# Performance work log

Hardware: AMD Instinct MI355X
Metric: run time of the kernel (lower is better)

## Reference

```python
import jax, jax.numpy as jnp
import numpy as np
import math

D_IN, D_MODEL, N_HEADS, N_LAYERS, D_FF = 128, 256, 4, 4, 1024
NUM_BANDS = D_MODEL // 6  # 42 -> 252 encoding dims, zero-padded to 256
LN_EPS = 1e-5


def setup_inputs() -> dict:
    key = jax.random.key(0)
    ks = jax.random.split(key, 32)
    N, B = 65536, 128
    s = 0.02
    L, D, F = N_LAYERS, D_MODEL, D_FF
    inp = {
        "dom_embeddings": jax.random.normal(ks[0], (N, D_IN), jnp.float32),
        "dom_to_event_idx": jnp.sort(jax.random.randint(ks[1], (N,), 0, B)),
        "batch_size": B,
        "geometry": jax.random.normal(ks[2], (N, 3), jnp.float32),
        "in_proj_w": jax.random.normal(ks[3], (D, D_IN), jnp.float32) * s,
        "in_proj_b": jnp.zeros((D,), jnp.float32),
        "geo_proj_w": jax.random.normal(ks[4], (D, D), jnp.float32) * s,
        "geo_proj_b": jnp.zeros((D,), jnp.float32),
        "cls_token": jax.random.normal(ks[5], (1, 1, D), jnp.float32),
        "qkv_w": jax.random.normal(ks[6], (L, 3 * D, D), jnp.float32) * s,
        "qkv_b": jnp.zeros((L, 3 * D), jnp.float32),
        "out_w": jax.random.normal(ks[7], (L, D, D), jnp.float32) * s,
        "out_b": jnp.zeros((L, D), jnp.float32),
        "ln1_w": jnp.ones((L, D), jnp.float32),
        "ln1_b": jnp.zeros((L, D), jnp.float32),
        "ln2_w": jnp.ones((L, D), jnp.float32),
        "ln2_b": jnp.zeros((L, D), jnp.float32),
        "ff_w1": jax.random.normal(ks[8], (L, F, D), jnp.float32) * s,
        "ff_b1": jnp.zeros((L, F), jnp.float32),
        "ff_w2": jax.random.normal(ks[9], (L, D, F), jnp.float32) * s,
        "ff_b2": jnp.zeros((L, D), jnp.float32),
        "head_w1": jax.random.normal(ks[10], (D, D), jnp.float32) * s,
        "head_b1": jnp.zeros((D,), jnp.float32),
        "head_w2": jax.random.normal(ks[11], (2, D), jnp.float32) * s,
        "head_b2": jnp.zeros((2,), jnp.float32),
    }
    return inp


def _layer_norm(x, w, b):
    m = x.mean(-1, keepdims=True)
    v = ((x - m) ** 2).mean(-1, keepdims=True)
    return (x - m) / jnp.sqrt(v + LN_EPS) * w + b


def _pos_enc(geometry):
    # geometry: (N,3). Order: per coord -> per freq -> [sin, cos]; pad to D_MODEL.
    freqs = jnp.logspace(0.0, 1.0, NUM_BANDS, dtype=jnp.float32)  # 1..max_freq=10
    ang = 2.0 * math.pi * geometry[:, :, None] * freqs[None, None, :]  # (N,3,F)
    sc = jnp.stack([jnp.sin(ang), jnp.cos(ang)], axis=-1)  # (N,3,F,2)
    enc = sc.reshape(geometry.shape[0], 3 * NUM_BANDS * 2)  # (N,252)
    pad = D_MODEL - enc.shape[1]
    return jnp.pad(enc, ((0, 0), (0, pad)))


def _self_attn(x, pad_mask, Wqkv, bqkv, Wo, bo):
    B, S, D = x.shape
    H, hd = N_HEADS, D // N_HEADS
    qkv = x @ Wqkv.T + bqkv  # (B,S,3D)
    q, k, v = jnp.split(qkv, 3, axis=-1)
    q = q.reshape(B, S, H, hd).transpose(0, 2, 1, 3)
    k = k.reshape(B, S, H, hd).transpose(0, 2, 1, 3)
    v = v.reshape(B, S, H, hd).transpose(0, 2, 1, 3)
    scores = jnp.einsum('bhqd,bhkd->bhqk', q, k) / math.sqrt(hd)
    scores = jnp.where(pad_mask[:, None, None, :], -jnp.inf, scores)
    a = jax.nn.softmax(scores, axis=-1)
    o = jnp.einsum('bhqk,bhkd->bhqd', a, v).transpose(0, 2, 1, 3).reshape(B, S, D)
    return o @ Wo.T + bo


def reference(dom_embeddings, dom_to_event_idx, batch_size, geometry,
              in_proj_w, in_proj_b, geo_proj_w, geo_proj_b, cls_token,
              qkv_w, qkv_b, out_w, out_b, ln1_w, ln1_b, ln2_w, ln2_b,
              ff_w1, ff_b1, ff_w2, ff_b2, head_w1, head_b1, head_w2, head_b2):
    N = dom_embeddings.shape[0]
    B = int(batch_size)
    x = dom_embeddings @ in_proj_w.T + in_proj_b  # (N,D)
    geo = _pos_enc(geometry) @ geo_proj_w.T + geo_proj_b
    x = x + geo

    # Vectorized scatter-pack (replaces per-DOM Python loop).
    counts = jnp.bincount(dom_to_event_idx, length=B)
    starts = jnp.concatenate([jnp.zeros((1,), counts.dtype), jnp.cumsum(counts)[:-1]])
    pos = jnp.arange(N) - starts[dom_to_event_idx] + 1  # slot 0 reserved for CLS
    max_doms = int(counts.max())
    S = max_doms + 1

    batch_tensor = jnp.zeros((B, S, D_MODEL), x.dtype)
    batch_tensor = batch_tensor.at[:, 0, :].set(cls_token[0, 0])
    batch_tensor = batch_tensor.at[dom_to_event_idx, pos].set(x)
    # True = padded. NOTE: CLS slot stays True, faithful to original code.
    pad_mask = jnp.ones((B, S), bool).at[dom_to_event_idx, pos].set(False)

    h = batch_tensor
    for l in range(N_LAYERS):  # pre-LN encoder layers
        h = h + _self_attn(_layer_norm(h, ln1_w[l], ln1_b[l]), pad_mask,
                           qkv_w[l], qkv_b[l], out_w[l], out_b[l])
        ff_in = _layer_norm(h, ln2_w[l], ln2_b[l])
        h = h + jax.nn.relu(ff_in @ ff_w1[l].T + ff_b1[l]) @ ff_w2[l].T + ff_b2[l]

    cls = h[:, 0, :]
    hid = jax.nn.relu(cls @ head_w1.T + head_b1)
    return hid @ head_w2.T + head_b2  # (B,2)
```

## Files before the change

### kernel.cpp

```cpp
#include <hip/hip_runtime.h>
#include <hip/hip_bf16.h>
#include <math.h>


#define D_INPUT  128
#define DM       256
#define NHEADS   4
#define HDIM     64
#define NLAYERS  4
#define DFF      1024
#define BEV      128
#define LNEPS    1e-5f
#define KT       10
#define SCL      0.18033688011112042f

typedef unsigned short u16;
typedef __attribute__((ext_vector_type(8))) short bf16x8;
typedef __attribute__((ext_vector_type(4))) float f32x4;

__device__ inline u16 f2bf(float x) {
    unsigned int xi = __float_as_uint(x);
    unsigned int r  = xi + 0x7FFFu + ((xi >> 16) & 1u);
    return (u16)(r >> 16);
}
__device__ inline unsigned int cvtpk(float lo, float hi) {
    unsigned int r;
    asm("v_cvt_pk_bf16_f32 %0, %1, %2" : "=v"(r) : "v"(lo), "v"(hi));
    return r;
}
__device__ inline void gload16(const void* g, void* l) {
    __builtin_amdgcn_global_load_lds(
        (const __attribute__((address_space(1))) unsigned int*)g,
        (__attribute__((address_space(3))) unsigned int*)l, 16, 0, 0);
}

__device__ inline size_t wpack_off(int col, int k, int nkt) {
    const int c16 = col >> 4, llo = col & 15;
    const int kt = k >> 6, kr = k & 63;
    const int kk = kr >> 5, lhi = (kr >> 3) & 3, e = kr & 7;
    return ((size_t)(c16 * nkt + kt)) * 1024 + kk * 512 + (lhi * 16 + llo) * 8 + e;
}


__global__ void starts_kernel(const int* __restrict__ idx, int* __restrict__ counts,
                              int* __restrict__ starts, int N) {
    __shared__ int bnd[BEV + 1];
    const int b = threadIdx.x;
    if (b <= BEV) {
        int lo = 0, hi = N;
        while (lo < hi) { int mid = (lo + hi) >> 1; if (idx[mid] < b) lo = mid + 1; else hi = mid; }
        bnd[b] = lo;
    }
    __syncthreads();
    if (b < BEV) { starts[b] = bnd[b]; counts[b] = bnd[b + 1] - bnd[b]; }
}

__global__ void r2bs_kernel(const int* __restrict__ idx, const int* __restrict__ starts,
                            int* __restrict__ r2bs, int N, int TP) {
    int i = blockIdx.x * blockDim.x + threadIdx.x;
    if (i < N) {
        int b = idx[i];
        r2bs[i] = (b << 16) | (i - starts[b] + 1);
    } else if (i < N + BEV) {
        r2bs[i] = (i - N) << 16;
    } else if (i < TP) {
        r2bs[i] = BEV << 16;
    }
}

__global__ void beacon_kernel(float* out, int n, float v) {
    int i = blockIdx.x * blockDim.x + threadIdx.x;
    if (i < n) out[i] = v;
}

__global__ void cvt4p_kernel(const float* __restrict__ s0, const float* __restrict__ s1,
                             const float* __restrict__ s2, const float* __restrict__ s3,
                             u16* __restrict__ d0, u16* __restrict__ d1,
                             u16* __restrict__ d2, u16* __restrict__ d3) {
    const int n0 = NLAYERS * 768 * 256, n1 = NLAYERS * 256 * 256;
    const int n2 = NLAYERS * 1024 * 256, n3 = NLAYERS * 256 * 1024;
    int i = blockIdx.x * blockDim.x + threadIdx.x;
    if (i < n0) {
        const int NoK = 768 * 256;
        int l = i / NoK, rem = i - l * NoK, col = rem >> 8, k = rem & 255;
        d0[(size_t)l * NoK + wpack_off(col, k, 4)] = f2bf(s0[i]);
        return;
    }
    i -= n0;
    if (i < n1) {
        const int NoK = 256 * 256;
        int l = i / NoK, rem = i - l * NoK, col = rem >> 8, k = rem & 255;
        d1[(size_t)l * NoK + wpack_off(col, k, 4)] = f2bf(s1[i]);
        return;
    }
    i -= n1;
    if (i < n2) {
        const int NoK = 1024 * 256;
        int l = i / NoK, rem = i - l * NoK, col = rem >> 8, k = rem & 255;
        d2[(size_t)l * NoK + wpack_off(col, k, 4)] = f2bf(s2[i]);
        return;
    }
    i -= n2;
    if (i < n3) {
        const int NoK = 256 * 1024;
        int l = i / NoK, rem = i - l * NoK, col = rem >> 10, k = rem & 1023;
        d3[(size_t)l * NoK + wpack_off(col, k, 16)] = f2bf(s3[i]);
    }
}

__global__ void prep_w_kernel(const float* __restrict__ win, const float* __restrict__ wgeo,
                              const float* __restrict__ bin, const float* __restrict__ bgeo,
                              u16* __restrict__ We, float* __restrict__ be) {
    int i = blockIdx.x * blockDim.x + threadIdx.x;
    if (i < 256 * 384) {
        int o = i / 384, k = i % 384;
        float v = 0.f;
        if (k < 128)      v = win[o * 128 + k];
        else if (k < 380) v = wgeo[o * 256 + (k - 128)];
        We[wpack_off(o, k, 6)] = f2bf(v);
    }
    if (i < 256) be[i] = bin[i] + bgeo[i];
}

__global__ void prep_a_kernel(const float* __restrict__ emb, const float* __restrict__ geo,
                              u16* __restrict__ A, int N) {
    size_t i = (size_t)blockIdx.x * blockDim.x + threadIdx.x;
    if (i >= (size_t)N * 384) return;
    int k = (int)(i % 384);
    size_t r = i / 384;
    float v = 0.f;
    if (k < 128) {
        v = emb[r * 128 + k];
    } else if (k < 380) {
        int rem  = k - 128;
        int axis = rem / 84;
        int r2   = rem % 84;
        int band = r2 >> 1;
        int sc   = r2 & 1;
        float freq = expf((float)band * (2.3025850929940457f / 41.0f));
        float ang  = (6.283185307179586f * geo[r * 3 + axis]) * freq;
        v = sc ? cosf(ang) : sinf(ang);
    }
    A[i] = f2bf(v);
}

__global__ void cls_kernel(const float* __restrict__ cls, float* __restrict__ h, int N) {
    h[(size_t)(N + blockIdx.x) * DM + threadIdx.x] = cls[threadIdx.x];
}


__global__ __launch_bounds__(256) void ln_kernel(const float* __restrict__ x,
                                                 const float* __restrict__ w,
                                                 const float* __restrict__ b,
                                                 u16* __restrict__ y, int T) {
    int row  = blockIdx.x * 4 + (threadIdx.x >> 6);
    int lane = threadIdx.x & 63;
    if (row >= T) return;
    float4 v = ((const float4*)(x + (size_t)row * DM))[lane];
    float s = v.x + v.y + v.z + v.w;
    #pragma unroll
    for (int off = 32; off > 0; off >>= 1) s += __shfl_xor(s, off);
    float mean = s * (1.0f / 256.0f);
    float dx = v.x - mean, dy = v.y - mean, dz = v.z - mean, dw = v.w - mean;
    float ss = dx * dx + dy * dy + dz * dz + dw * dw;
    #pragma unroll
    for (int off = 32; off > 0; off >>= 1) ss += __shfl_xor(ss, off);
    float inv = rsqrtf(ss * (1.0f / 256.0f) + LNEPS);
    float4 wv = ((const float4*)w)[lane];
    float4 bv = ((const float4*)b)[lane];
    ushort4 o;
    o.x = f2bf(dx * inv * wv.x + bv.x);
    o.y = f2bf(dy * inv * wv.y + bv.y);
    o.z = f2bf(dz * inv * wv.z + bv.z);
    o.w = f2bf(dw * inv * wv.w + bv.w);
    ((ushort4*)(y + (size_t)row * DM))[lane] = o;
}


template <typename OutT>
__global__ __launch_bounds__(512) void mgemm_kernel(const u16* __restrict__ A,
                                                    const u16* __restrict__ Wp,
                                                    const float* __restrict__ bias,
                                                    OutT* __restrict__ C,
                                                    int K, int No, int ldc, int flags,
                                                    const int* __restrict__ r2bs,
                                                    u16* __restrict__ KVt) {
    __shared__ u16 As[256 * 64];
    const int m0 = blockIdx.y * 256, n0 = blockIdx.x * 128;
    const int tid  = threadIdx.x;
    const int w    = tid >> 6, lane = tid & 63;
    const int wr   = w >> 1,  wc   = w & 1;
    const int lhi  = lane >> 4, llo = lane & 15;
    const int nkt  = K >> 6;

    f32x4 acc[4][4];
    #pragma unroll
    for (int i = 0; i < 4; ++i)
        #pragma unroll
        for (int j = 0; j < 4; ++j) acc[i][j] = (f32x4){0.f, 0.f, 0.f, 0.f};

    for (int kt = 0; kt < K; kt += 64) {
        __syncthreads();
        #pragma unroll
        for (int it = 0; it < 4; ++it) {
            int un = it * 512 + tid;
            int r = un >> 3, c8 = un & 7;
            gload16(A + (size_t)(m0 + r) * K + kt + ((c8 ^ (r & 7)) * 8), &As[un * 8]);
        }
        __syncthreads();
        const u16* wb = Wp + ((size_t)(kt >> 6)) * 1024 + lane * 8;
        #pragma unroll
        for (int kk = 0; kk < 2; ++kk) {
            bf16x8 af[4], bfr[4];
            #pragma unroll
            for (int i = 0; i < 4; ++i) {
                const int row = wr * 64 + i * 16 + llo;
                af[i] = *(const bf16x8*)&As[row * 64 + (((kk * 4 + lhi) ^ (row & 7)) * 8)];
            }
            #pragma unroll
            for (int j = 0; j < 4; ++j) {
                const int c16 = (n0 >> 4) + wc * 4 + j;
                bfr[j] = *(const bf16x8*)(wb + ((size_t)c16 * nkt) * 1024 + kk * 512);
            }
            #pragma unroll
            for (int i = 0; i < 4; ++i)
                #pragma unroll
                for (int j = 0; j < 4; ++j)
                    acc[i][j] = __builtin_amdgcn_mfma_f32_16x16x32_bf16(af[i], bfr[j], acc[i][j], 0, 0, 0);
        }
    }

    const int vmode = (flags & 4) ? (n0 >= 512 ? 2 : (n0 >= 256 ? 1 : 0)) : 0;
    #pragma unroll
    for (int i = 0; i < 4; ++i) {
        const int row0 = m0 + wr * 64 + i * 16 + lhi * 4;
        int bsr[4];
        if (vmode) {
            #pragma unroll
            for (int r = 0; r < 4; ++r) bsr[r] = r2bs[row0 + r];
        }
        #pragma unroll
        for (int j = 0; j < 4; ++j) {
            const int col = n0 + wc * 64 + j * 16 + llo;
            const float bb = bias[col];
            if (vmode == 1) {
                const int hh = (col - 256) >> 6, d = (col - 256) & 63;
                const int kk_t = d >> 5, lhi_t = (d >> 3) & 3, e = d & 7;
                #pragma unroll
                for (int r = 0; r < 4; ++r) {
                    const int eb = bsr[r] >> 16, pos = bsr[r] & 0xffff;
                    const int ktile = pos >> 6;
                    if (ktile < KT) {
                        const int unit = ((pos & 63) >> 4) * 2 + kk_t;
                        const int lane_t = lhi_t * 16 + (pos & 15);
                        KVt[(((size_t)(eb * 4 + hh) * 2 + 0) * KT + ktile) * 4096
                            + unit * 512 + lane_t * 8 + e] = f2bf(acc[i][j][r] + bb);
                    }
                }
            } else if (vmode == 2) {
                const int hh = (col - 512) >> 6, d = (col - 512) & 63;
                const int i_t = d >> 4, llo_t = d & 15;
                #pragma unroll
                for (int r = 0; r < 4; ++r) {
                    const int eb = bsr[r] >> 16, pos = bsr[r] & 0xffff;
                    const int ktile = pos >> 6;
                    if (ktile < KT) {
                        const int unit = i_t * 2 + ((pos & 63) >> 5);
                        const int lane_t = (((pos & 63) >> 3) & 3) * 16 + llo_t;
                        KVt[(((size_t)(eb * 4 + hh) * 2 + 1) * KT + ktile) * 4096
                            + unit * 512 + lane_t * 8 + (pos & 7)] = f2bf(acc[i][j][r] + bb);
                    }
                }
            } else {
                #pragma unroll
                for (int r = 0; r < 4; ++r) {
                    float v = acc[i][j][r] + bb;
                    if ((flags & 8) && col < 256) v *= SCL;
                    size_t idx = (size_t)(row0 + r) * ldc + col;
                    if constexpr (sizeof(OutT) == 4) {
                        float* cp = (float*)C + idx;
                        if (flags & 2) v += *cp;
                        if (flags & 1) v = fmaxf(v, 0.f);
                        *cp = v;
                    } else {
                        if (flags & 1) v = fmaxf(v, 0.f);
                        ((u16*)C)[idx] = f2bf(v);
                    }
                }
            }
        }
    }
}


__global__ __launch_bounds__(256) void mgemmln_kernel(const u16* __restrict__ X,
                                                      const u16* __restrict__ Wp,
                                                      const float* __restrict__ bias,
                                                      float* __restrict__ H,
                                                      const float* __restrict__ lnw,
                                                      const float* __restrict__ lnb,
                                                      u16* __restrict__ Y,
                                                      int K) {
    __shared__ u16 Xs[64 * 64];
    __shared__ float part[2][4][64];
    const int m0 = blockIdx.x * 64;
    const int tid = threadIdx.x;
    const int wc = tid >> 6, lane = tid & 63;
    const int lhi = lane >> 4, llo = lane & 15;
    const int nkt = K >> 6;

    f32x4 acc[4][4];
    #pragma unroll
    for (int i = 0; i < 4; ++i)
        #pragma unroll
        for (int j = 0; j < 4; ++j) acc[i][j] = (f32x4){0.f, 0.f, 0.f, 0.f};

    for (int kt = 0; kt < K; kt += 64) {
        __syncthreads();
        #pragma unroll
        for (int it = 0; it < 2; ++it) {
            int un = it * 256 + tid;
            int r = un >> 3, c8 = un & 7;
            gload16(X + (size_t)(m0 + r) * K + kt + ((c8 ^ (r & 7)) * 8), &Xs[un * 8]);
        }
        __syncthreads();
        const u16* wb = Wp + ((size_t)(kt >> 6)) * 1024 + lane * 8;
        #pragma unroll
        for (int kk = 0; kk < 2; ++kk) {
            bf16x8 xf[4], wf[4];
            #pragma unroll
            for (int i = 0; i < 4; ++i) {
                const int row = i * 16 + llo;
                xf[i] = *(const bf16x8*)&Xs[row * 64 + (((kk * 4 + lhi) ^ (row & 7)) * 8)];
            }
            #pragma unroll
            for (int j = 0; j < 4; ++j) {
                const int c16 = wc * 4 + j;
                wf[j] = *(const bf16x8*)(wb + ((size_t)c16 * nkt) * 1024 + kk * 512);
            }
            #pragma unroll
            for (int i = 0; i < 4; ++i)
                #pragma unroll
                for (int j = 0; j < 4; ++j)
                    acc[i][j] = __builtin_amdgcn_mfma_f32_16x16x32_bf16(wf[j], xf[i], acc[i][j], 0, 0, 0);
        }
    }

    float rsum[4], rsq[4];
    #pragma unroll
    for (int i = 0; i < 4; ++i) { rsum[i] = 0.f; rsq[i] = 0.f; }
    #pragma unroll
    for (int i = 0; i < 4; ++i) {
        const int row = m0 + i * 16 + llo;
        #pragma unroll
        for (int j = 0; j < 4; ++j) {
            const int col0 = wc * 64 + j * 16 + lhi * 4;
            const float4 bb = *(const float4*)&bias[col0];
            const float4 hv = *(const float4*)&H[(size_t)row * DM + col0];
            float v0 = acc[i][j][0] + bb.x + hv.x;
            float v1 = acc[i][j][1] + bb.y + hv.y;
            float v2 = acc[i][j][2] + bb.z + hv.z;
            float v3 = acc[i][j][3] + bb.w + hv.w;
            acc[i][j][0] = v0; acc[i][j][1] = v1; acc[i][j][2] = v2; acc[i][j][3] = v3;
            rsum[i] += (v0 + v1) + (v2 + v3);
            rsq[i]  += (v0 * v0 + v1 * v1) + (v2 * v2 + v3 * v3);
        }
    }
    #pragma unroll
    for (int i = 0; i < 4; ++i) {
        rsum[i] += __shfl_xor(rsum[i], 16);  rsum[i] += __shfl_xor(rsum[i], 32);
        rsq[i]  += __shfl_xor(rsq[i], 16);   rsq[i]  += __shfl_xor(rsq[i], 32);
    }
    __syncthreads();
    if (lhi == 0) {
        #pragma unroll
        for (int i = 0; i < 4; ++i) {
            const int rl = i * 16 + llo;
            part[0][wc][rl] = rsum[i];
            part[1][wc][rl] = rsq[i];
        }
    }
    __syncthreads();

    #pragma unroll
    for (int i = 0; i < 4; ++i) {
        const int rl = i * 16 + llo;
        const int row = m0 + rl;
        const float s = (part[0][0][rl] + part[0][1][rl]) + (part[0][2][rl] + part[0][3][rl]);
        const float q = (part[1][0][rl] + part[1][1][rl]) + (part[1][2][rl] + part[1][3][rl]);
        const float mean = s * (1.0f / 256.0f);
        const float var  = fmaxf(q * (1.0f / 256.0f) - mean * mean, 0.f);
        const float rstd = rsqrtf(var + LNEPS);
        #pragma unroll
        for (int j = 0; j < 4; ++j) {
            const int col0 = wc * 64 + j * 16 + lhi * 4;
            const float4 wv = *(const float4*)&lnw[col0];
            const float4 bv = *(const float4*)&lnb[col0];
            float4 hv;
            hv.x = acc[i][j][0]; hv.y = acc[i][j][1];
            hv.z = acc[i][j][2]; hv.w = acc[i][j][3];
            *(float4*)&H[(size_t)row * DM + col0] = hv;
            uint2 yy;
            yy.x = cvtpk((hv.x - mean) * rstd * wv.x + bv.x,
                         (hv.y - mean) * rstd * wv.y + bv.y);
            yy.y = cvtpk((hv.z - mean) * rstd * wv.z + bv.z,
                         (hv.w - mean) * rstd * wv.w + bv.w);
            *(uint2*)&Y[(size_t)row * DM + col0] = yy;
        }
    }
}


__global__ __launch_bounds__(256) void mattn_kernel(const u16* __restrict__ Qb,
                                                    const u16* __restrict__ KVt,
                                                    const int* __restrict__ counts,
                                                    const int* __restrict__ starts,
                                                    u16* __restrict__ out, int N) {
    const int id  = blockIdx.x;
    const int rem = id >> 3;
    const int qt  = rem % KT;
    const int bh  = (rem / KT) * 8 + (id & 7);
    const int b = bh >> 2, hh = bh & 3;
    const int Sb = counts[b] + 1;
    const int qbase = qt * 64;
    if (qbase >= Sb) return;
    const int start = starts[b];
    __shared__ u16 Pl[4][16 * 72];
    const int tid = threadIdx.x;
    const int w = tid >> 6, lane = tid & 63;
    const int llo = lane & 15, lhi = lane >> 4;

    const int qi = qbase + w * 16 + llo;
    const size_t qrow = (qi < Sb && qi > 0) ? (size_t)(start + qi - 1) : (size_t)(N + b);
    bf16x8 bq[2];
    bq[0] = *(const bf16x8*)(Qb + qrow * 256 + hh * 64 + lhi * 8);
    bq[1] = *(const bf16x8*)(Qb + qrow * 256 + hh * 64 + 32 + lhi * 8);

    const u16* kb = KVt + ((size_t)bh * 2 + 0) * KT * 4096;
    const u16* vb = KVt + ((size_t)bh * 2 + 1) * KT * 4096;

    f32x4 acc[4];
    #pragma unroll
    for (int i = 0; i < 4; ++i) acc[i] = (f32x4){0.f, 0.f, 0.f, 0.f};
    float m = -1e30f, l = 0.f;

    int nt = (Sb + 63) >> 6;
    if (nt > KT) nt = KT;

    for (int t = 0; t < nt; ++t) {
        const int kbase = t * 64;
        const u16* kp = kb + t * 4096 + lane * 8;
        const u16* vp = vb + t * 4096 + lane * 8;

        bf16x8 ak[4][2], av[4][2];
        #pragma unroll
        for (int i = 0; i < 4; ++i) {
            #pragma unroll
            for (int kk = 0; kk < 2; ++kk) {
                ak[i][kk] = *(const bf16x8*)(kp + (i * 2 + kk) * 512);
                av[i][kk] = *(const bf16x8*)(vp + (i * 2 + kk) * 512);
            }
        }

        f32x4 sc[4];
        #pragma unroll
        for (int i = 0; i < 4; ++i) sc[i] = (f32x4){0.f, 0.f, 0.f, 0.f};
        #pragma unroll
        for (int kk = 0; kk < 2; ++kk)
            #pragma unroll
            for (int i = 0; i < 4; ++i)
                sc[i] = __builtin_amdgcn_mfma_f32_16x16x32_bf16(ak[i][kk], bq[kk], sc[i], 0, 0, 0);

        float rm;
        if (kbase + 64 <= Sb) {
            float m0v = fmaxf(fmaxf(sc[0][0], sc[0][1]), fmaxf(sc[0][2], sc[0][3]));
            float m1v = fmaxf(fmaxf(sc[1][0], sc[1][1]), fmaxf(sc[1][2], sc[1][3]));
            float m2v = fmaxf(fmaxf(sc[2][0], sc[2][1]), fmaxf(sc[2][2], sc[2][3]));
            float m3v = fmaxf(fmaxf(sc[3][0], sc[3][1]), fmaxf(sc[3][2], sc[3][3]));
            rm = fmaxf(fmaxf(m0v, m1v), fmaxf(m2v, m3v));
        } else {
            rm = -1e30f;
            #pragma unroll
            for (int i = 0; i < 4; ++i)
                #pragma unroll
                for (int r = 0; r < 4; ++r) {
                    const int key = kbase + i * 16 + lhi * 4 + r;
                    const float s = (key < Sb) ? sc[i][r] : -1e30f;
                    sc[i][r] = s;
                    rm = fmaxf(rm, s);
                }
        }
        rm = fmaxf(rm, __shfl_xor(rm, 16));
        rm = fmaxf(rm, __shfl_xor(rm, 32));

        if (!__all(rm <= m + 8.f)) {
            const float mnew = fmaxf(m, rm);
            const float corr = exp2f(m - mnew);
            l *= corr;
            #pragma unroll
            for (int i = 0; i < 4; ++i) acc[i] *= corr;
            m = mnew;
        }

        float ls = 0.f;
        #pragma unroll
        for (int i = 0; i < 4; ++i) {
            const float p0 = exp2f(sc[i][0] - m), p1 = exp2f(sc[i][1] - m);
            const float p2 = exp2f(sc[i][2] - m), p3 = exp2f(sc[i][3] - m);
            ls += (p0 + p1) + (p2 + p3);
            uint2 pp;
            pp.x = cvtpk(p0, p1);
            pp.y = cvtpk(p2, p3);
            *(uint2*)&Pl[w][llo * 72 + i * 16 + lhi * 4] = pp;
        }
        ls += __shfl_xor(ls, 16);
        ls += __shfl_xor(ls, 32);
        l += ls;

        #pragma unroll
        for (int kk = 0; kk < 2; ++kk) {
            bf16x8 pb = *(const bf16x8*)&Pl[w][llo * 72 + kk * 32 + lhi * 8];
            #pragma unroll
            for (int i = 0; i < 4; ++i)
                acc[i] = __builtin_amdgcn_mfma_f32_16x16x32_bf16(av[i][kk], pb, acc[i], 0, 0, 0);
        }
    }

    if (qi < Sb) {
        const size_t orow = (qi == 0) ? (size_t)(N + b) : (size_t)(start + qi - 1);
        const float invl = 1.f / l;
        #pragma unroll
        for (int i = 0; i < 4; ++i) {
            ushort4 o;
            o.x = f2bf(acc[i][0] * invl);
            o.y = f2bf(acc[i][1] * invl);
            o.z = f2bf(acc[i][2] * invl);
            o.w = f2bf(acc[i][3] * invl);
            *(ushort4*)&out[orow * DM + hh * HDIM + i * 16 + lhi * 4] = o;
        }
    }
}


__global__ __launch_bounds__(256) void head_kernel(const float* __restrict__ h,
                                                   const float* __restrict__ w1,
                                                   const float* __restrict__ b1,
                                                   const float* __restrict__ w2,
                                                   const float* __restrict__ b2,
                                                   float* __restrict__ out, int N) {
    const int b = blockIdx.x;
    const int t = threadIdx.x;
    __shared__ float cls[DM];
    __shared__ float hid[DM];
    cls[t] = h[(size_t)(N + b) * DM + t];
    __syncthreads();
    float s = b1[t];
    for (int k = 0; k < DM; ++k) s = fmaf(cls[k], w1[t * DM + k], s);
    hid[t] = fmaxf(s, 0.f);
    __syncthreads();
    if (t < 2) {
        float o = b2[t];
        for (int k = 0; k < DM; ++k) o = fmaf(hid[k], w2[t * DM + k], o);
        out[b * 2 + t] = o;
    }
}


extern "C" void kernel_launch(void* const* d_in, const int* in_sizes, int n_in,
                              void* d_out, int out_size, void* d_ws, size_t ws_size,
                              hipStream_t stream) {
    const float* dom_emb   = (const float*)d_in[0];
    const int*   dom_idx   = (const int*)d_in[1];
    const float* geometry  = (const float*)d_in[3];
    const float* in_w      = (const float*)d_in[4];
    const float* in_b      = (const float*)d_in[5];
    const float* geo_w     = (const float*)d_in[6];
    const float* geo_b     = (const float*)d_in[7];
    const float* cls_tok   = (const float*)d_in[8];
    const float* qkv_w     = (const float*)d_in[9];
    const float* qkv_b     = (const float*)d_in[10];
    const float* out_w     = (const float*)d_in[11];
    const float* out_b     = (const float*)d_in[12];
    const float* ln1_w     = (const float*)d_in[13];
    const float* ln1_b     = (const float*)d_in[14];
    const float* ln2_w     = (const float*)d_in[15];
    const float* ln2_b     = (const float*)d_in[16];
    const float* ff_w1     = (const float*)d_in[17];
    const float* ff_b1     = (const float*)d_in[18];
    const float* ff_w2     = (const float*)d_in[19];
    const float* ff_b2     = (const float*)d_in[20];
    const float* head_w1   = (const float*)d_in[21];
    const float* head_b1   = (const float*)d_in[22];
    const float* head_w2   = (const float*)d_in[23];
    const float* head_b2   = (const float*)d_in[24];
    float* outp = (float*)d_out;

    const int N  = in_sizes[0] / D_INPUT;
    const int T  = N + BEV;
    const int TP = ((T + 255) / 256) * 256;

    char* base = (char*)d_ws;
    size_t off = 0;
    int* counts = (int*)(base + off);          off += 1024;
    int* starts = (int*)(base + off);          off += 1024;
    u16*   Web  = (u16*)(base + off);          off += (size_t)256 * 384 * 2;
    float* be   = (float*)(base + off);        off += 1024;
    u16*   wq   = (u16*)(base + off);          off += (size_t)NLAYERS * 768 * 256 * 2;
    u16*   wo   = (u16*)(base + off);          off += (size_t)NLAYERS * 256 * 256 * 2;
    u16*   w1b  = (u16*)(base + off);          off += (size_t)NLAYERS * 1024 * 256 * 2;
    u16*   w2b  = (u16*)(base + off);          off += (size_t)NLAYERS * 256 * 1024 * 2;
    int*   r2bs = (int*)(base + off);          off += ((size_t)TP * 4 + 255) & ~255ULL;
    float* h    = (float*)(base + off);        off += (size_t)TP * DM * 4;
    u16*   xb   = (u16*)(base + off);          off += (size_t)TP * DM * 2;
    const size_t qb_sz  = (size_t)TP * 256 * 2;
    const size_t kvt_sz = (size_t)(BEV + 1) * 4 * 2 * KT * 4096 * 2;
    const size_t big2   = qb_sz + kvt_sz;
    const size_t ff1_sz = (size_t)TP * 1024 * 2;
    char* bigc = base + off;
    const bool ff_single = ws_size >= off + (ff1_sz > big2 ? ff1_sz : big2);
    off += ff_single ? (ff1_sz > big2 ? ff1_sz : big2) : big2;

    u16* Ab   = (u16*)bigc;
    u16* Qbuf = (u16*)bigc;
    u16* KVt  = (u16*)(bigc + qb_sz);
    u16* ffm  = (u16*)bigc;

    if (ws_size < off) {
        beacon_kernel<<<1, 256, 0, stream>>>(outp, out_size, (float)(ws_size >> 20));
        return;
    }

    {
        const int ntot = NLAYERS * (768 * 256 + 256 * 256 + 1024 * 256 + 256 * 1024);
        cvt4p_kernel<<<(ntot + 255) / 256, 256, 0, stream>>>(
            qkv_w, out_w, ff_w1, ff_w2, wq, wo, w1b, w2b);
    }
    prep_w_kernel<<<(256 * 384 + 255) / 256, 256, 0, stream>>>(in_w, geo_w, in_b, geo_b, Web, be);

    starts_kernel<<<1, 256, 0, stream>>>(dom_idx, counts, starts, N);
    r2bs_kernel<<<(TP + 255) / 256, 256, 0, stream>>>(dom_idx, starts, r2bs, N, TP);

    prep_a_kernel<<<(int)(((size_t)N * 384 + 255) / 256), 256, 0, stream>>>(dom_emb, geometry, Ab, N);
    mgemm_kernel<float><<<dim3(2, N / 256), 512, 0, stream>>>(
        Ab, Web, be, h, 384, DM, DM, 0, nullptr, nullptr);
    cls_kernel<<<BEV, DM, 0, stream>>>(cls_tok, h, N);

    const int MT = TP / 256;
    int chs[2], nch;
    if (ff_single) { chs[0] = MT; nch = 1; }
    else           { chs[0] = (MT + 1) / 2; chs[1] = MT - chs[0]; nch = 2; }
    ln_kernel<<<TP / 4, 256, 0, stream>>>(h, ln1_w, ln1_b, xb, TP);
    for (int l = 0; l < NLAYERS; ++l) {
        mgemm_kernel<u16><<<dim3(6, MT), 512, 0, stream>>>(
            xb, wq + (size_t)l * 768 * 256, qkv_b + l * 768, Qbuf, 256, 768, 256, 4 | 8,
            r2bs, KVt);
        mattn_kernel<<<8 * KT * (BEV * NHEADS / 8), 256, 0, stream>>>(
            Qbuf, KVt, counts, starts, xb, N);
        mgemmln_kernel<<<TP / 64, 256, 0, stream>>>(
            xb, wo + (size_t)l * 256 * 256, out_b + l * DM, h,
            ln2_w + l * DM, ln2_b + l * DM, xb, 256);
        const int lnx = (l + 1 < NLAYERS) ? (l + 1) : l;
        int t0 = 0;
        for (int c = 0; c < nch; ++c) {
            const size_t r0 = (size_t)t0 * 256;
            mgemm_kernel<u16><<<dim3(8, chs[c]), 512, 0, stream>>>(
                xb + r0 * DM, w1b + (size_t)l * DFF * 256, ff_b1 + l * DFF, ffm,
                256, DFF, DFF, 1, nullptr, nullptr);
            mgemmln_kernel<<<chs[c] * 4, 256, 0, stream>>>(
                ffm, w2b + (size_t)l * 256 * DFF, ff_b2 + l * DM, h + r0 * DM,
                ln1_w + lnx * DM, ln1_b + lnx * DM, xb + r0 * DM, DFF);
            t0 += chs[c];
        }
    }

    head_kernel<<<BEV, DM, 0, stream>>>(h, head_w1, head_b1, head_w2, head_b2, outp, N);
}
```

Baseline: 1.762 ms.

## Pre-pack activations in MFMA tile layout and fuse the feed-forward block into one kernel

Activations are now written straight into the MFMA fragment-packed layout (apack), so the GEMMs read fragments directly from global memory and no longer stage tiles through LDS or synchronise around them. The FF1 and FF2 GEMMs are fused into one kernel that keeps the 1024-wide intermediate on chip, which removes the large round trip of the intermediate buffer and the chunking logic. The QKV GEMM is rewritten with smaller row tiles and vectorised epilogue stores, the input kernel packs four values per thread, and attention MFMA sections get s_setprio hints. Dropping LDS staging puts more load on L2/global bandwidth, and the fused FF kernel may have lower occupancy.

Measured after the change: 2.805 ms. 1.59x slower.

```diff
diff --git a/kernel.cpp b/kernel.cpp
--- a/kernel.cpp
+++ b/kernel.cpp
@@ -28,12 +28,12 @@
     asm("v_cvt_pk_bf16_f32 %0, %1, %2" : "=v"(r) : "v"(lo), "v"(hi));
     return r;
 }
-__device__ inline void gload16(const void* g, void* l) {
-    __builtin_amdgcn_global_load_lds(
-        (const __attribute__((address_space(1))) unsigned int*)g,
-        (__attribute__((address_space(3))) unsigned int*)l, 16, 0, 0);
-}
-
+
+__device__ inline size_t apack(int row, int col, int nkt) {
+    return ((size_t)(row >> 4) * nkt + (col >> 6)) * 1024
+         + ((col >> 5) & 1) * 512
+         + ((((col >> 3) & 3) * 16 + (row & 15)) * 8) + (col & 7);
+}
 __device__ inline size_t wpack_off(int col, int k, int nkt) {
     const int c16 = col >> 4, llo = col & 15;
     const int kt = k >> 6, kr = k & 63;
@@ -123,25 +123,34 @@
 }
 
 __global__ void prep_a_kernel(const float* __restrict__ emb, const float* __restrict__ geo,
-                              u16* __restrict__ A, int N) {
-    size_t i = (size_t)blockIdx.x * blockDim.x + threadIdx.x;
-    if (i >= (size_t)N * 384) return;
-    int k = (int)(i % 384);
-    size_t r = i / 384;
-    float v = 0.f;
-    if (k < 128) {
-        v = emb[r * 128 + k];
-    } else if (k < 380) {
-        int rem  = k - 128;
-        int axis = rem / 84;
-        int r2   = rem % 84;
-        int band = r2 >> 1;
-        int sc   = r2 & 1;
-        float freq = expf((float)band * (2.3025850929940457f / 41.0f));
-        float ang  = (6.283185307179586f * geo[r * 3 + axis]) * freq;
-        v = sc ? cosf(ang) : sinf(ang);
-    }
-    A[i] = f2bf(v);
+                              u16* __restrict__ Ap, int N) {
+    size_t t = (size_t)blockIdx.x * blockDim.x + threadIdx.x;
+    if (t >= (size_t)N * 96) return;
+    const int c4 = (int)(t % 96) * 4;
+    const size_t r = t / 96;
+    float v[4];
+    #pragma unroll
+    for (int u = 0; u < 4; ++u) {
+        const int k = c4 + u;
+        float x = 0.f;
+        if (k < 128) {
+            x = emb[r * 128 + k];
+        } else if (k < 380) {
+            int rem  = k - 128;
+            int axis = rem / 84;
+            int r2   = rem % 84;
+            int band = r2 >> 1;
+            int sc   = r2 & 1;
+            float freq = expf((float)band * (2.3025850929940457f / 41.0f));
+            float ang  = (6.283185307179586f * geo[r * 3 + axis]) * freq;
+            x = sc ? cosf(ang) : sinf(ang);
+        }
+        v[u] = x;
+    }
+    uint2 pp;
+    pp.x = cvtpk(v[0], v[1]);
+    pp.y = cvtpk(v[2], v[3]);
+    *(uint2*)&Ap[apack((int)r, c4, 6)] = pp;
 }
 
 __global__ void cls_kernel(const float* __restrict__ cls, float* __restrict__ h, int N) {
@@ -152,7 +161,7 @@
 __global__ __launch_bounds__(256) void ln_kernel(const float* __restrict__ x,
                                                  const float* __restrict__ w,
                                                  const float* __restrict__ b,
-                                                 u16* __restrict__ y, int T) {
+                                                 u16* __restrict__ yp, int T) {
     int row  = blockIdx.x * 4 + (threadIdx.x >> 6);
     int lane = threadIdx.x & 63;
     if (row >= T) return;
@@ -168,30 +177,27 @@
     float inv = rsqrtf(ss * (1.0f / 256.0f) + LNEPS);
     float4 wv = ((const float4*)w)[lane];
     float4 bv = ((const float4*)b)[lane];
-    ushort4 o;
-    o.x = f2bf(dx * inv * wv.x + bv.x);
-    o.y = f2bf(dy * inv * wv.y + bv.y);
-    o.z = f2bf(dz * inv * wv.z + bv.z);
-    o.w = f2bf(dw * inv * wv.w + bv.w);
-    ((ushort4*)(y + (size_t)row * DM))[lane] = o;
-}
-
-
-template <typename OutT>
-__global__ __launch_bounds__(512) void mgemm_kernel(const u16* __restrict__ A,
+    const int col0 = lane * 4;
+    uint2 yy;
+    yy.x = cvtpk(dx * inv * wv.x + bv.x, dy * inv * wv.y + bv.y);
+    yy.y = cvtpk(dz * inv * wv.z + bv.z, dw * inv * wv.w + bv.w);
+    *(uint2*)&yp[apack(row, col0, 4)] = yy;
+}
+
+
+template <int MODE>
+__global__ __launch_bounds__(256) void pgemm_kernel(const u16* __restrict__ Xp,
                                                     const u16* __restrict__ Wp,
                                                     const float* __restrict__ bias,
-                                                    OutT* __restrict__ C,
-                                                    int K, int No, int ldc, int flags,
+                                                    float* __restrict__ C,
+                                                    u16* __restrict__ Qb,
+                                                    u16* __restrict__ KVt,
                                                     const int* __restrict__ r2bs,
-                                                    u16* __restrict__ KVt) {
-    __shared__ u16 As[256 * 64];
-    const int m0 = blockIdx.y * 256, n0 = blockIdx.x * 128;
-    const int tid  = threadIdx.x;
-    const int w    = tid >> 6, lane = tid & 63;
-    const int wr   = w >> 1,  wc   = w & 1;
-    const int lhi  = lane >> 4, llo = lane & 15;
-    const int nkt  = K >> 6;
+                                                    int nkt) {
+    const int m0 = blockIdx.y * 64, n0 = blockIdx.x * 256;
+    const int tid = threadIdx.x, wv = tid >> 6, lane = tid & 63;
+    const int lhi = lane >> 4, llo = lane & 15;
+    const int rt0 = m0 >> 4;
 
     f32x4 acc[4][4];
     #pragma unroll
@@ -199,93 +205,69 @@
         #pragma unroll
         for (int j = 0; j < 4; ++j) acc[i][j] = (f32x4){0.f, 0.f, 0.f, 0.f};
 
-    for (int kt = 0; kt < K; kt += 64) {
-        __syncthreads();
-        #pragma unroll
-        for (int it = 0; it < 4; ++it) {
-            int un = it * 512 + tid;
-            int r = un >> 3, c8 = un & 7;
-            gload16(A + (size_t)(m0 + r) * K + kt + ((c8 ^ (r & 7)) * 8), &As[un * 8]);
-        }
-        __syncthreads();
-        const u16* wb = Wp + ((size_t)(kt >> 6)) * 1024 + lane * 8;
+    for (int kt = 0; kt < nkt; ++kt) {
         #pragma unroll
         for (int kk = 0; kk < 2; ++kk) {
-            bf16x8 af[4], bfr[4];
-            #pragma unroll
-            for (int i = 0; i < 4; ++i) {
-                const int row = wr * 64 + i * 16 + llo;
-                af[i] = *(const bf16x8*)&As[row * 64 + (((kk * 4 + lhi) ^ (row & 7)) * 8)];
-            }
+            bf16x8 xf[4], wf[4];
+            #pragma unroll
+            for (int i = 0; i < 4; ++i)
+                xf[i] = *(const bf16x8*)(Xp + ((size_t)(rt0 + i) * nkt + kt) * 1024
+                                         + kk * 512 + lane * 8);
             #pragma unroll
             for (int j = 0; j < 4; ++j) {
-                const int c16 = (n0 >> 4) + wc * 4 + j;
-                bfr[j] = *(const bf16x8*)(wb + ((size_t)c16 * nkt) * 1024 + kk * 512);
+                const int c16 = (n0 >> 4) + wv * 4 + j;
+                wf[j] = *(const bf16x8*)(Wp + ((size_t)c16 * nkt + kt) * 1024
+                                         + kk * 512 + lane * 8);
             }
             #pragma unroll
             for (int i = 0; i < 4; ++i)
                 #pragma unroll
                 for (int j = 0; j < 4; ++j)
-                    acc[i][j] = __builtin_amdgcn_mfma_f32_16x16x32_bf16(af[i], bfr[j], acc[i][j], 0, 0, 0);
-        }
-    }
-
-    const int vmode = (flags & 4) ? (n0 >= 512 ? 2 : (n0 >= 256 ? 1 : 0)) : 0;
+                    acc[i][j] = __builtin_amdgcn_mfma_f32_16x16x32_bf16(wf[j], xf[i], acc[i][j], 0, 0, 0);
+        }
+    }
+
     #pragma unroll
     for (int i = 0; i < 4; ++i) {
-        const int row0 = m0 + wr * 64 + i * 16 + lhi * 4;
-        int bsr[4];
-        if (vmode) {
-            #pragma unroll
-            for (int r = 0; r < 4; ++r) bsr[r] = r2bs[row0 + r];
+        const int row = m0 + i * 16 + llo;
+        int eb = 0, pos = 0, ktile = KT;
+        if (MODE == 1 && n0 >= 256) {
+            const int bs = r2bs[row];
+            eb = bs >> 16; pos = bs & 0xffff; ktile = pos >> 6;
         }
         #pragma unroll
         for (int j = 0; j < 4; ++j) {
-            const int col = n0 + wc * 64 + j * 16 + llo;
-            const float bb = bias[col];
-            if (vmode == 1) {
-                const int hh = (col - 256) >> 6, d = (col - 256) & 63;
-                const int kk_t = d >> 5, lhi_t = (d >> 3) & 3, e = d & 7;
-                #pragma unroll
-                for (int r = 0; r < 4; ++r) {
-                    const int eb = bsr[r] >> 16, pos = bsr[r] & 0xffff;
-                    const int ktile = pos >> 6;
-                    if (ktile < KT) {
-                        const int unit = ((pos & 63) >> 4) * 2 + kk_t;
-                        const int lane_t = lhi_t * 16 + (pos & 15);
-                        KVt[(((size_t)(eb * 4 + hh) * 2 + 0) * KT + ktile) * 4096
-                            + unit * 512 + lane_t * 8 + e] = f2bf(acc[i][j][r] + bb);
-                    }
-                }
-            } else if (vmode == 2) {
-                const int hh = (col - 512) >> 6, d = (col - 512) & 63;
-                const int i_t = d >> 4, llo_t = d & 15;
-                #pragma unroll
-                for (int r = 0; r < 4; ++r) {
-                    const int eb = bsr[r] >> 16, pos = bsr[r] & 0xffff;
-                    const int ktile = pos >> 6;
-                    if (ktile < KT) {
-                        const int unit = i_t * 2 + ((pos & 63) >> 5);
-                        const int lane_t = (((pos & 63) >> 3) & 3) * 16 + llo_t;
-                        KVt[(((size_t)(eb * 4 + hh) * 2 + 1) * KT + ktile) * 4096
-                            + unit * 512 + lane_t * 8 + (pos & 7)] = f2bf(acc[i][j][r] + bb);
-                    }
+            const int col0 = n0 + wv * 64 + j * 16 + lhi * 4;
+            const float4 bb = *(const float4*)&bias[col0];
+            const float v0 = acc[i][j][0] + bb.x, v1 = acc[i][j][1] + bb.y;
+            const float v2 = acc[i][j][2] + bb.z, v3 = acc[i][j][3] + bb.w;
+            if (MODE == 0) {
+                float4 c = {v0, v1, v2, v3};
+                *(float4*)&C[(size_t)row * 256 + col0] = c;
+            } else if (n0 == 0) {
+                uint2 q;
+                q.x = cvtpk(v0 * SCL, v1 * SCL);
+                q.y = cvtpk(v2 * SCL, v3 * SCL);
+                *(uint2*)&Qb[(size_t)row * 256 + col0] = q;
+            } else if (n0 == 256) {
+                if (ktile < KT) {
+                    const int dg = col0 - 256, hh = dg >> 6, d0 = dg & 63;
+                    const int unit = ((pos & 63) >> 4) * 2 + (d0 >> 5);
+                    const int lt = ((d0 >> 3) & 3) * 16 + (pos & 15);
+                    uint2 pp = {cvtpk(v0, v1), cvtpk(v2, v3)};
+                    *(uint2*)&KVt[(((size_t)(eb * 4 + hh) * 2 + 0) * KT + ktile) * 4096
+                                  + unit * 512 + lt * 8 + (d0 & 7)] = pp;
                 }
             } else {
-                #pragma unroll
-                for (int r = 0; r < 4; ++r) {
-                    float v = acc[i][j][r] + bb;
-                    if ((flags & 8) && col < 256) v *= SCL;
-                    size_t idx = (size_t)(row0 + r) * ldc + col;
-                    if constexpr (sizeof(OutT) == 4) {
-                        float* cp = (float*)C + idx;
-                        if (flags & 2) v += *cp;
-                        if (flags & 1) v = fmaxf(v, 0.f);
-                        *cp = v;
-                    } else {
-                        if (flags & 1) v = fmaxf(v, 0.f);
-                        ((u16*)C)[idx] = f2bf(v);
-                    }
+                if (ktile < KT) {
+                    const int dg = col0 - 512, hh = dg >> 6, d0 = dg & 63;
+                    const size_t vb = (((size_t)(eb * 4 + hh) * 2 + 1) * KT + ktile) * 4096
+                                    + ((d0 >> 4) * 2 + ((pos & 63) >> 5)) * 512
+                                    + ((((pos & 63) >> 3) & 3) * 16) * 8 + (pos & 7);
+                    KVt[vb + (size_t)((d0 & 15) + 0) * 8] = f2bf(v0);
+                    KVt[vb + (size_t)((d0 & 15) + 1) * 8] = f2bf(v1);
+                    KVt[vb + (size_t)((d0 & 15) + 2) * 8] = f2bf(v2);
+                    KVt[vb + (size_t)((d0 & 15) + 3) * 8] = f2bf(v3);
                 }
             }
         }
@@ -293,21 +275,19 @@
 }
 
 
-__global__ __launch_bounds__(256) void mgemmln_kernel(const u16* __restrict__ X,
+__global__ __launch_bounds__(256) void mgemmln_kernel(const u16* __restrict__ Xp,
                                                       const u16* __restrict__ Wp,
                                                       const float* __restrict__ bias,
                                                       float* __restrict__ H,
                                                       const float* __restrict__ lnw,
                                                       const float* __restrict__ lnb,
-                                                      u16* __restrict__ Y,
-                                                      int K) {
-    __shared__ u16 Xs[64 * 64];
+                                                      u16* __restrict__ Yp,
+                                                      int nkt) {
     __shared__ float part[2][4][64];
     const int m0 = blockIdx.x * 64;
-    const int tid = threadIdx.x;
-    const int wc = tid >> 6, lane = tid & 63;
+    const int tid = threadIdx.x, wv = tid >> 6, lane = tid & 63;
     const int lhi = lane >> 4, llo = lane & 15;
-    const int nkt = K >> 6;
+    const int rt0 = m0 >> 4;
 
     f32x4 acc[4][4];
     #pragma unroll
@@ -315,28 +295,19 @@
         #pragma unroll
         for (int j = 0; j < 4; ++j) acc[i][j] = (f32x4){0.f, 0.f, 0.f, 0.f};
 
-    for (int kt = 0; kt < K; kt += 64) {
-        __syncthreads();
-        #pragma unroll
-        for (int it = 0; it < 2; ++it) {
-            int un = it * 256 + tid;
-            int r = un >> 3, c8 = un & 7;
-            gload16(X + (size_t)(m0 + r) * K + kt + ((c8 ^ (r & 7)) * 8), &Xs[un * 8]);
-        }
-        __syncthreads();
-        const u16* wb = Wp + ((size_t)(kt >> 6)) * 1024 + lane * 8;
+    for (int kt = 0; kt < nkt; ++kt) {
         #pragma unroll
         for (int kk = 0; kk < 2; ++kk) {
             bf16x8 xf[4], wf[4];
             #pragma unroll
-            for (int i = 0; i < 4; ++i) {
-                const int row = i * 16 + llo;
-                xf[i] = *(const bf16x8*)&Xs[row * 64 + (((kk * 4 + lhi) ^ (row & 7)) * 8)];
-            }
+            for (int i = 0; i < 4; ++i)
+                xf[i] = *(const bf16x8*)(Xp + ((size_t)(rt0 + i) * nkt + kt) * 1024
+                                         + kk * 512 + lane * 8);
             #pragma unroll
             for (int j = 0; j < 4; ++j) {
-                const int c16 = wc * 4 + j;
-                wf[j] = *(const bf16x8*)(wb + ((size_t)c16 * nkt) * 1024 + kk * 512);
+                const int c16 = wv * 4 + j;
+                wf[j] = *(const bf16x8*)(Wp + ((size_t)c16 * nkt + kt) * 1024
+                                         + kk * 512 + lane * 8);
             }
             #pragma unroll
             for (int i = 0; i < 4; ++i)
@@ -354,7 +325,7 @@
         const int row = m0 + i * 16 + llo;
         #pragma unroll
         for (int j = 0; j < 4; ++j) {
-            const int col0 = wc * 64 + j * 16 + lhi * 4;
+            const int col0 = wv * 64 + j * 16 + lhi * 4;
             const float4 bb = *(const float4*)&bias[col0];
             const float4 hv = *(const float4*)&H[(size_t)row * DM + col0];
             float v0 = acc[i][j][0] + bb.x + hv.x;
@@ -376,8 +347,8 @@
         #pragma unroll
         for (int i = 0; i < 4; ++i) {
             const int rl = i * 16 + llo;
-            part[0][wc][rl] = rsum[i];
-            part[1][wc][rl] = rsq[i];
+            part[0][wv][rl] = rsum[i];
+            part[1][wv][rl] = rsq[i];
         }
     }
     __syncthreads();
@@ -393,19 +364,163 @@
         const float rstd = rsqrtf(var + LNEPS);
         #pragma unroll
         for (int j = 0; j < 4; ++j) {
-            const int col0 = wc * 64 + j * 16 + lhi * 4;
-            const float4 wv = *(const float4*)&lnw[col0];
-            const float4 bv = *(const float4*)&lnb[col0];
+            const int col0 = wv * 64 + j * 16 + lhi * 4;
+            const float4 wl = *(const float4*)&lnw[col0];
+            const float4 bl = *(const float4*)&lnb[col0];
             float4 hv;
             hv.x = acc[i][j][0]; hv.y = acc[i][j][1];
             hv.z = acc[i][j][2]; hv.w = acc[i][j][3];
             *(float4*)&H[(size_t)row * DM + col0] = hv;
             uint2 yy;
-            yy.x = cvtpk((hv.x - mean) * rstd * wv.x + bv.x,
-                         (hv.y - mean) * rstd * wv.y + bv.y);
-            yy.y = cvtpk((hv.z - mean) * rstd * wv.z + bv.z,
-                         (hv.w - mean) * rstd * wv.w + bv.w);
-            *(uint2*)&Y[(size_t)row * DM + col0] = yy;
+            yy.x = cvtpk((hv.x - mean) * rstd * wl.x + bl.x,
+                         (hv.y - mean) * rstd * wl.y + bl.y);
+            yy.y = cvtpk((hv.z - mean) * rstd * wl.z + bl.z,
+                         (hv.w - mean) * rstd * wl.w + bl.w);
+            *(uint2*)&Yp[apack(row, col0, 4)] = yy;
+        }
+    }
+}
+
+
+__global__ __launch_bounds__(512) void fusedff_kernel(const u16* __restrict__ Xp,
+                                                      const u16* __restrict__ W1p,
+                                                      const float* __restrict__ b1,
+                                                      const u16* __restrict__ W2p,
+                                                      const float* __restrict__ b2,
+                                                      float* __restrict__ H,
+                                                      const float* __restrict__ lnw,
+                                                      const float* __restrict__ lnb,
+                                                      u16* __restrict__ Yp) {
+    __shared__ u16 mid[8 * 8 * 2 * 512];
+    __shared__ float part[2][8][128];
+    const int m0 = blockIdx.x * 128;
+    const int tid = threadIdx.x, wv = tid >> 6, lane = tid & 63;
+    const int lhi = lane >> 4, llo = lane & 15;
+    const int rt0 = m0 >> 4;
+
+    f32x4 oacc[8][2];
+    #pragma unroll
+    for (int i = 0; i < 8; ++i)
+        #pragma unroll
+        for (int j = 0; j < 2; ++j) oacc[i][j] = (f32x4){0.f, 0.f, 0.f, 0.f};
+
+    for (int h2 = 0; h2 < 2; ++h2) {
+        for (int j2 = 0; j2 < 4; ++j2) {
+            const int c16 = h2 * 32 + wv * 4 + j2;
+            f32x4 acc[8];
+            #pragma unroll
+            for (int i = 0; i < 8; ++i) acc[i] = (f32x4){0.f, 0.f, 0.f, 0.f};
+            for (int kt = 0; kt < 4; ++kt) {
+                const u16* wb = W1p + ((size_t)(c16 * 4 + kt)) * 1024 + lane * 8;
+                #pragma unroll
+                for (int kk = 0; kk < 2; ++kk) {
+                    bf16x8 wf = *(const bf16x8*)(wb + kk * 512);
+                    #pragma unroll
+                    for (int i = 0; i < 8; ++i) {
+                        bf16x8 xf = *(const bf16x8*)(Xp + ((size_t)(rt0 + i) * 4 + kt) * 1024
+                                                     + kk * 512 + lane * 8);
+                        acc[i] = __builtin_amdgcn_mfma_f32_16x16x32_bf16(wf, xf, acc[i], 0, 0, 0);
+                    }
+                }
+            }
+            const int colbase = c16 * 16 + lhi * 4;
+            const float4 bb = *(const float4*)&b1[colbase];
+            const int mtH = (colbase >> 6) - h2 * 8;
+            const int kk2 = (colbase >> 5) & 1;
+            const int lt  = ((colbase >> 3) & 3) * 16 + llo;
+            const int e0  = colbase & 7;
+            #pragma unroll
+            for (int i = 0; i < 8; ++i) {
+                const float v0 = fmaxf(acc[i][0] + bb.x, 0.f);
+                const float v1 = fmaxf(acc[i][1] + bb.y, 0.f);
+                const float v2 = fmaxf(acc[i][2] + bb.z, 0.f);
+                const float v3 = fmaxf(acc[i][3] + bb.w, 0.f);
+                uint2 pp = {cvtpk(v0, v1), cvtpk(v2, v3)};
+                *(uint2*)&mid[((i * 8 + mtH) * 2 + kk2) * 512 + lt * 8 + e0] = pp;
+            }
+        }
+        __syncthreads();
+        for (int mtH = 0; mtH < 8; ++mtH) {
+            #pragma unroll
+            for (int kk = 0; kk < 2; ++kk) {
+                bf16x8 mf[8];
+                #pragma unroll
+                for (int i = 0; i < 8; ++i)
+                    mf[i] = *(const bf16x8*)&mid[((i * 8 + mtH) * 2 + kk) * 512 + lane * 8];
+                #pragma unroll
+                for (int j = 0; j < 2; ++j) {
+                    const int c16o = wv * 2 + j;
+                    bf16x8 wf = *(const bf16x8*)(W2p + ((size_t)(c16o * 16 + h2 * 8 + mtH)) * 1024
+                                                 + kk * 512 + lane * 8);
+                    #pragma unroll
+                    for (int i = 0; i < 8; ++i)
+                        oacc[i][j] = __builtin_amdgcn_mfma_f32_16x16x32_bf16(wf, mf[i], oacc[i][j], 0, 0, 0);
+                }
+            }
+        }
+        __syncthreads();
+    }
+
+    float rsum[8], rsq[8];
+    #pragma unroll
+    for (int i = 0; i < 8; ++i) { rsum[i] = 0.f; rsq[i] = 0.f; }
+    #pragma unroll
+    for (int i = 0; i < 8; ++i) {
+        const int row = m0 + i * 16 + llo;
+        #pragma unroll
+        for (int j = 0; j < 2; ++j) {
+            const int col0 = wv * 32 + j * 16 + lhi * 4;
+            const float4 bb = *(const float4*)&b2[col0];
+            const float4 hv = *(const float4*)&H[(size_t)row * DM + col0];
+            float v0 = oacc[i][j][0] + bb.x + hv.x;
+            float v1 = oacc[i][j][1] + bb.y + hv.y;
+            float v2 = oacc[i][j][2] + bb.z + hv.z;
+            float v3 = oacc[i][j][3] + bb.w + hv.w;
+            oacc[i][j][0] = v0; oacc[i][j][1] = v1; oacc[i][j][2] = v2; oacc[i][j][3] = v3;
+            rsum[i] += (v0 + v1) + (v2 + v3);
+            rsq[i]  += (v0 * v0 + v1 * v1) + (v2 * v2 + v3 * v3);
+        }
+    }
+    #pragma unroll
+    for (int i = 0; i < 8; ++i) {
+        rsum[i] += __shfl_xor(rsum[i], 16);  rsum[i] += __shfl_xor(rsum[i], 32);
+        rsq[i]  += __shfl_xor(rsq[i], 16);   rsq[i]  += __shfl_xor(rsq[i], 32);
+    }
+    if (lhi == 0) {
+        #pragma unroll
+        for (int i = 0; i < 8; ++i) {
+            const int rl = i * 16 + llo;
+            part[0][wv][rl] = rsum[i];
+            part[1][wv][rl] = rsq[i];
+        }
+    }
+    __syncthreads();
+
+    #pragma unroll
+    for (int i = 0; i < 8; ++i) {
+        const int rl = i * 16 + llo;
+        const int row = m0 + rl;
+        float s = 0.f, q = 0.f;
+        #pragma unroll
+        for (int w2 = 0; w2 < 8; ++w2) { s += part[0][w2][rl]; q += part[1][w2][rl]; }
+        const float mean = s * (1.0f / 256.0f);
+        const float var  = fmaxf(q * (1.0f / 256.0f) - mean * mean, 0.f);
+        const float rstd = rsqrtf(var + LNEPS);
+        #pragma unroll
+        for (int j = 0; j < 2; ++j) {
+            const int col0 = wv * 32 + j * 16 + lhi * 4;
+            const float4 wl = *(const float4*)&lnw[col0];
+            const float4 bl = *(const float4*)&lnb[col0];
+            float4 hv;
+            hv.x = oacc[i][j][0]; hv.y = oacc[i][j][1];
+            hv.z = oacc[i][j][2]; hv.w = oacc[i][j][3];
+            *(float4*)&H[(size_t)row * DM + col0] = hv;
+            uint2 yy;
+            yy.x = cvtpk((hv.x - mean) * rstd * wl.x + bl.x,
+                         (hv.y - mean) * rstd * wl.y + bl.y);
+            yy.y = cvtpk((hv.z - mean) * rstd * wl.z + bl.z,
+                         (hv.w - mean) * rstd * wl.w + bl.w);
+            *(uint2*)&Yp[apack(row, col0, 4)] = yy;
         }
     }
 }
@@ -415,7 +530,7 @@
                                                     const u16* __restrict__ KVt,
                                                     const int* __restrict__ counts,
                                                     const int* __restrict__ starts,
-                                                    u16* __restrict__ out, int N) {
+                                                    u16* __restrict__ outp, int N) {
     const int id  = blockIdx.x;
     const int rem = id >> 3;
     const int qt  = rem % KT;
@@ -465,11 +580,13 @@
         f32x4 sc[4];
         #pragma unroll
         for (int i = 0; i < 4; ++i) sc[i] = (f32x4){0.f, 0.f, 0.f, 0.f};
+        __builtin_amdgcn_s_setprio(1);
         #pragma unroll
         for (int kk = 0; kk < 2; ++kk)
             #pragma unroll
             for (int i = 0; i < 4; ++i)
                 sc[i] = __builtin_amdgcn_mfma_f32_16x16x32_bf16(ak[i][kk], bq[kk], sc[i], 0, 0, 0);
+        __builtin_amdgcn_s_setprio(0);
 
         float rm;
         if (kbase + 64 <= Sb) {
@@ -517,6 +634,7 @@
         ls += __shfl_xor(ls, 32);
         l += ls;
 
+        __builtin_amdgcn_s_setprio(1);
         #pragma unroll
         for (int kk = 0; kk < 2; ++kk) {
             bf16x8 pb = *(const bf16x8*)&Pl[w][llo * 72 + kk * 32 + lhi * 8];
@@ -524,6 +642,7 @@
             for (int i = 0; i < 4; ++i)
                 acc[i] = __builtin_amdgcn_mfma_f32_16x16x32_bf16(av[i][kk], pb, acc[i], 0, 0, 0);
         }
+        __builtin_amdgcn_s_setprio(0);
     }
 
     if (qi < Sb) {
@@ -531,12 +650,11 @@
         const float invl = 1.f / l;
         #pragma unroll
         for (int i = 0; i < 4; ++i) {
-            ushort4 o;
-            o.x = f2bf(acc[i][0] * invl);
-            o.y = f2bf(acc[i][1] * invl);
-            o.z = f2bf(acc[i][2] * invl);
-            o.w = f2bf(acc[i][3] * invl);
-            *(ushort4*)&out[orow * DM + hh * HDIM + i * 16 + lhi * 4] = o;
+            const int col0 = hh * 64 + i * 16 + lhi * 4;
+            uint2 yy;
+            yy.x = cvtpk(acc[i][0] * invl, acc[i][1] * invl);
+            yy.y = cvtpk(acc[i][2] * invl, acc[i][3] * invl);
+            *(uint2*)&outp[apack((int)orow, col0, 4)] = yy;
         }
     }
 }
@@ -614,16 +732,10 @@
     u16*   xb   = (u16*)(base + off);          off += (size_t)TP * DM * 2;
     const size_t qb_sz  = (size_t)TP * 256 * 2;
     const size_t kvt_sz = (size_t)(BEV + 1) * 4 * 2 * KT * 4096 * 2;
-    const size_t big2   = qb_sz + kvt_sz;
-    const size_t ff1_sz = (size_t)TP * 1024 * 2;
-    char* bigc = base + off;
-    const bool ff_single = ws_size >= off + (ff1_sz > big2 ? ff1_sz : big2);
-    off += ff_single ? (ff1_sz > big2 ? ff1_sz : big2) : big2;
-
+    char* bigc = base + off;                   off += qb_sz + kvt_sz;
     u16* Ab   = (u16*)bigc;
     u16* Qbuf = (u16*)bigc;
     u16* KVt  = (u16*)(bigc + qb_sz);
-    u16* ffm  = (u16*)bigc;
 
     if (ws_size < off) {
         beacon_kernel<<<1, 256, 0, stream>>>(outp, out_size, (float)(ws_size >> 20));
@@ -640,37 +752,25 @@
     starts_kernel<<<1, 256, 0, stream>>>(dom_idx, counts, starts, N);
     r2bs_kernel<<<(TP + 255) / 256, 256, 0, stream>>>(dom_idx, starts, r2bs, N, TP);
 
-    prep_a_kernel<<<(int)(((size_t)N * 384 + 255) / 256), 256, 0, stream>>>(dom_emb, geometry, Ab, N);
-    mgemm_kernel<float><<<dim3(2, N / 256), 512, 0, stream>>>(
-        Ab, Web, be, h, 384, DM, DM, 0, nullptr, nullptr);
+    prep_a_kernel<<<(int)(((size_t)N * 96 + 255) / 256), 256, 0, stream>>>(dom_emb, geometry, Ab, N);
+    pgemm_kernel<0><<<dim3(1, N / 64), 256, 0, stream>>>(
+        Ab, Web, be, h, nullptr, nullptr, nullptr, 6);
     cls_kernel<<<BEV, DM, 0, stream>>>(cls_tok, h, N);
 
-    const int MT = TP / 256;
-    int chs[2], nch;
-    if (ff_single) { chs[0] = MT; nch = 1; }
-    else           { chs[0] = (MT + 1) / 2; chs[1] = MT - chs[0]; nch = 2; }
     ln_kernel<<<TP / 4, 256, 0, stream>>>(h, ln1_w, ln1_b, xb, TP);
     for (int l = 0; l < NLAYERS; ++l) {
-        mgemm_kernel<u16><<<dim3(6, MT), 512, 0, stream>>>(
-            xb, wq + (size_t)l * 768 * 256, qkv_b + l * 768, Qbuf, 256, 768, 256, 4 | 8,
-            r2bs, KVt);
+        pgemm_kernel<1><<<dim3(3, TP / 64), 256, 0, stream>>>(
+            xb, wq + (size_t)l * 768 * 256, qkv_b + l * 768, nullptr, Qbuf, KVt, r2bs, 4);
         mattn_kernel<<<8 * KT * (BEV * NHEADS / 8), 256, 0, stream>>>(
             Qbuf, KVt, counts, starts, xb, N);
         mgemmln_kernel<<<TP / 64, 256, 0, stream>>>(
             xb, wo + (size_t)l * 256 * 256, out_b + l * DM, h,
-            ln2_w + l * DM, ln2_b + l * DM, xb, 256);
+            ln2_w + l * DM, ln2_b + l * DM, xb, 4);
         const int lnx = (l + 1 < NLAYERS) ? (l + 1) : l;
-        int t0 = 0;
-        for (int c = 0; c < nch; ++c) {
-            const size_t r0 = (size_t)t0 * 256;
-            mgemm_kernel<u16><<<dim3(8, chs[c]), 512, 0, stream>>>(
-                xb + r0 * DM, w1b + (size_t)l * DFF * 256, ff_b1 + l * DFF, ffm,
-                256, DFF, DFF, 1, nullptr, nullptr);
-            mgemmln_kernel<<<chs[c] * 4, 256, 0, stream>>>(
-                ffm, w2b + (size_t)l * 256 * DFF, ff_b2 + l * DM, h + r0 * DM,
-                ln1_w + lnx * DM, ln1_b + lnx * DM, xb + r0 * DM, DFF);
-            t0 += chs[c];
-        }
+        fusedff_kernel<<<TP / 128, 512, 0, stream>>>(
+            xb, w1b + (size_t)l * DFF * 256, ff_b1 + l * DFF,
+            w2b + (size_t)l * 256 * DFF, ff_b2 + l * DM, h,
+            ln1_w + lnx * DM, ln1_b + lnx * DM, xb);
     }
 
     head_kernel<<<BEV, DM, 0, stream>>>(h, head_w1, head_b1, head_w2, head_b2, outp, N);
```
